# Optimization experiments

Hardware: AMD Instinct MI355X
Metric: run time of the kernel (lower is better)

## Reference

```python
import jax, jax.numpy as jnp
import numpy as np
from jax import lax

B, L, D, C = 4096, 50, 128, 64
V = 100000
H = D // 2  # bidirectional LSTM hidden size; 2*H == emb_dim


def setup_inputs() -> dict:
    key = jax.random.key(0)
    ks = jax.random.split(key, 26)
    f = lambda k, s: jax.random.normal(k, s, dtype=jnp.float32) * 0.05
    return {
        "r_idx": jax.random.randint(ks[0], (B,), 0, V),
        "a_idx": jax.random.randint(ks[1], (B,), 0, V),
        "acc_idx": jax.random.randint(ks[2], (B,), 0, V),
        "rank_q": jax.random.normal(ks[3], (B, L, D), dtype=jnp.float32),
        "rank_q_len": jax.random.randint(ks[4], (B,), 0, L),
        "ru_emb": f(ks[5], (V, D)),
        "au_emb": f(ks[6], (V, D)),
        "Wih_f": f(ks[7], (4 * H, D)), "Whh_f": f(ks[8], (4 * H, H)),
        "bih_f": f(ks[9], (4 * H,)), "bhh_f": f(ks[10], (4 * H,)),
        "Wih_b": f(ks[11], (4 * H, D)), "Whh_b": f(ks[12], (4 * H, H)),
        "bih_b": f(ks[13], (4 * H,)), "bhh_b": f(ks[14], (4 * H,)),
        "conv1_w": f(ks[15], (C, 1, D)), "conv1_b": f(ks[16], (C,)),
        "conv2_w": f(ks[17], (C, 2, D)), "conv2_b": f(ks[18], (C,)),
        "conv3_w": f(ks[19], (C, 3, D)), "conv3_b": f(ks[20], (C,)),
        "fc1_w": f(ks[21], (6,)), "fc1_b": f(ks[22], (1,)),
        "fc2_w": f(ks[23], (C,)), "fc2_b": f(ks[24], (1,)),
    }


def _lstm_dir(x, Wih, Whh, bih, bhh, reverse):
    # x: [B, L, D] -> outputs [B, L, H]; PyTorch gate order i,f,g,o
    b = x.shape[0]
    xs = jnp.swapaxes(x, 0, 1)  # [L, B, D]
    h0 = jnp.zeros((b, Whh.shape[1]), x.dtype)

    def step(carry, xt):
        h, c = carry
        gates = xt @ Wih.T + h @ Whh.T + (bih + bhh)
        i, fg, g, o = jnp.split(gates, 4, axis=-1)
        i = jax.nn.sigmoid(i)
        fg = jax.nn.sigmoid(fg)
        g = jnp.tanh(g)
        o = jax.nn.sigmoid(o)
        c = fg * c + i * g
        h = o * jnp.tanh(c)
        return (h, c), h

    _, ys = lax.scan(step, (h0, h0), xs, reverse=reverse)
    return jnp.swapaxes(ys, 0, 1)


def _score(mat, conv1_w, conv1_b, conv2_w, conv2_b, conv3_w, conv3_b, fc1_w, fc1_b, fc2_w, fc2_b):
    # mat: [B, 3, D]; three tiny conv branches (kernel heights 1/2/3, width=D)
    branches = []
    for w, bias in ((conv1_w, conv1_b), (conv2_w, conv2_b), (conv3_w, conv3_b)):
        k = w.shape[1]
        wins = jnp.stack([mat[:, i:i + k] for i in range(3 - k + 1)], axis=1)  # [B, W, k, D]
        branches.append(jax.nn.relu(jnp.einsum('bwkd,ckd->bcw', wins, w) + bias[None, :, None]))
    s = jnp.concatenate(branches, axis=2)  # [B, C, 6]
    h = jnp.einsum('bcw,w->bc', s, fc1_w) + fc1_b[0]  # fc_new_1: 6 -> 1
    return jnp.einsum('bc,c->b', h, fc2_w) + fc2_b[0]  # fc_new_2: C -> 1


def reference(r_idx, a_idx, acc_idx, rank_q, rank_q_len, ru_emb, au_emb,
              Wih_f, Whh_f, bih_f, bhh_f, Wih_b, Whh_b, bih_b, bhh_b,
              conv1_w, conv1_b, conv2_w, conv2_b, conv3_w, conv3_b,
              fc1_w, fc1_b, fc2_w, fc2_b):
    emb_r = ru_emb[r_idx]
    emb_a = au_emb[a_idx]
    emb_acc = au_emb[acc_idx]
    # bidirectional LSTM over the question sequence
    out_f = _lstm_dir(rank_q, Wih_f, Whh_f, bih_f, bhh_f, reverse=False)
    out_b = _lstm_dir(rank_q, Wih_b, Whh_b, bih_b, bhh_b, reverse=True)
    q_out = jnp.concatenate([out_f, out_b], axis=-1)  # [B, L, D]
    # prepend a zero timestep, then gather per-example at index rank_q_len
    q_pad = jnp.concatenate([jnp.zeros((q_out.shape[0], 1, q_out.shape[2]), q_out.dtype), q_out], axis=1)
    emb_q = q_pad[jnp.arange(q_pad.shape[0]), rank_q_len]  # [B, D]
    low = jnp.stack([emb_r, emb_q, emb_a], axis=1)   # [B, 3, D]
    high = jnp.stack([emb_r, emb_q, emb_acc], axis=1)
    fcp = (conv1_w, conv1_b, conv2_w, conv2_b, conv3_w, conv3_b, fc1_w, fc1_b, fc2_w, fc2_b)
    low_s = _score(low, *fcp)
    high_s = _score(high, *fcp)
    return jnp.sum(low_s - high_s)
```

## Files before the change

### kernel.cpp

```cpp
#include <hip/hip_runtime.h>
#include <hip/hip_bf16.h>

#define LSEQ 50
#define BATCH 4096

typedef __attribute__((ext_vector_type(8))) short bf16x8;
typedef __attribute__((ext_vector_type(4))) float f32x4;

__device__ __forceinline__ unsigned cvtpk(float lo, float hi) {
    unsigned r;
    asm("v_cvt_pk_bf16_f32 %0, %1, %2" : "=v"(r) : "v"(lo), "v"(hi));
    return r;
}
__device__ __forceinline__ bf16x8 pack8(float4 a, float4 b) {
    uint4 u;
    u.x = cvtpk(a.x, a.y); u.y = cvtpk(a.z, a.w);
    u.z = cvtpk(b.x, b.y); u.w = cvtpk(b.z, b.w);
    return __builtin_bit_cast(bf16x8, u);
}
__device__ __forceinline__ float fsigm(float x) {
    return __builtin_amdgcn_rcpf(1.0f + __builtin_amdgcn_exp2f(-1.44269504f * x));
}
__device__ __forceinline__ float ftanh(float x) {
    float e = __builtin_amdgcn_exp2f(2.88539008f * x);
    return 1.0f - 2.0f * __builtin_amdgcn_rcpf(e + 1.0f);
}

__global__ __launch_bounds__(256, 2)
void lstm_kernel(const float* __restrict__ rank_q, const int* __restrict__ qlen,
                 const float* __restrict__ Wih_f, const float* __restrict__ Whh_f,
                 const float* __restrict__ bih_f, const float* __restrict__ bhh_f,
                 const float* __restrict__ Wih_b, const float* __restrict__ Whh_b,
                 const float* __restrict__ bih_b, const float* __restrict__ bhh_b,
                 float* __restrict__ embq)
{
    const int blk = blockIdx.x;
    const int dir = blk >> 8;
    const int b0  = (blk & 255) << 4;
    const int tid = threadIdx.x;
    const int wv  = tid >> 6;
    const int ln  = tid & 63;
    const int lm  = ln & 15;
    const int lq  = ln >> 4;
    const int m   = (wv << 4) + lm;

    const float* Wih = dir ? Wih_b : Wih_f;
    const float* Whh = dir ? Whh_b : Whh_f;
    const float* bih = dir ? bih_b : bih_f;
    const float* bhh = dir ? bhh_b : bhh_f;

    __shared__ __align__(16) unsigned short xbuf[4][16][136];
    __shared__ __align__(16) unsigned short hbuf[2][16][72];

    bf16x8 bfrag[4][6];
    float bias[4];
    #pragma unroll
    for (int j = 0; j < 4; ++j) {
        const int n = (j << 6) + m;
        bias[j] = bih[n] + bhh[n];
        #pragma unroll
        for (int s = 0; s < 6; ++s) {
            const int kb = (s << 5) + (lq << 3);
            const float* src = (s < 4) ? (Wih + n * 128 + kb)
                                       : (Whh + n * 64 + (kb - 128));
            bfrag[j][s] = pack8(*(const float4*)src, *(const float4*)(src + 4));
        }
    }

    int len_e[4];
    #pragma unroll
    for (int r = 0; r < 4; ++r) len_e[r] = qlen[b0 + (lq << 2) + r];

    float cst[4]  = {0.f, 0.f, 0.f, 0.f};
    float qval[4] = {0.f, 0.f, 0.f, 0.f};

    for (int i = tid; i < 16 * 72; i += 256) ((unsigned short*)hbuf)[i] = 0;

    const int se = tid >> 4;
    const int sd = (tid & 15) << 3;
    const int tstep = dir ? -128 : 128;
    const float* gp = rank_q + ((size_t)(b0 + se) * LSEQ + (dir ? LSEQ - 1 : 0)) * 128 + sd;

    float4 p0a = *(const float4*)gp, p0b = *(const float4*)(gp + 4); gp += tstep;
    float4 p1a = *(const float4*)gp, p1b = *(const float4*)(gp + 4); gp += tstep;
    float4 p2a = *(const float4*)gp, p2b = *(const float4*)(gp + 4); gp += tstep;
    float4 p3a = *(const float4*)gp, p3b = *(const float4*)(gp + 4); gp += tstep;
    float4 fa0 = *(const float4*)gp, fa1 = *(const float4*)(gp + 4); gp += tstep;
    float4 fb0 = *(const float4*)gp, fb1 = *(const float4*)(gp + 4); gp += tstep;
    *(bf16x8*)&xbuf[0][se][sd] = pack8(p0a, p0b);
    *(bf16x8*)&xbuf[1][se][sd] = pack8(p1a, p1b);
    *(bf16x8*)&xbuf[2][se][sd] = pack8(p2a, p2b);
    *(bf16x8*)&xbuf[3][se][sd] = pack8(p3a, p3b);
    __syncthreads();

    const int xoff = lm * 136 + (lq << 3);
    const int hoff = lm * 72 + (lq << 3);

    f32x4 accx[4];
    {
        const unsigned short* xb = &xbuf[0][0][0];
        bf16x8 x0 = *(const bf16x8*)(xb + xoff);
        bf16x8 x1 = *(const bf16x8*)(xb + xoff + 32);
        bf16x8 x2 = *(const bf16x8*)(xb + xoff + 64);
        bf16x8 x3 = *(const bf16x8*)(xb + xoff + 96);
        #pragma unroll
        for (int j = 0; j < 4; ++j) {
            f32x4 a = {bias[j], bias[j], bias[j], bias[j]};
            a = __builtin_amdgcn_mfma_f32_16x16x32_bf16(x0, bfrag[j][0], a, 0, 0, 0);
            a = __builtin_amdgcn_mfma_f32_16x16x32_bf16(x1, bfrag[j][1], a, 0, 0, 0);
            a = __builtin_amdgcn_mfma_f32_16x16x32_bf16(x2, bfrag[j][2], a, 0, 0, 0);
            a = __builtin_amdgcn_mfma_f32_16x16x32_bf16(x3, bfrag[j][3], a, 0, 0, 0);
            accx[j] = a;
        }
    }

#define LSTM_BODY(T, FS0, FS1)                                                  \
    {                                                                           \
        const int t  = (T);                                                     \
        const int rb = t & 1, wb = rb ^ 1;                                      \
             \
        if (t + 4 < LSEQ) *(bf16x8*)&xbuf[t & 3][se][sd] = pack8(FS0, FS1);     \
                \
        if (t + 6 < LSEQ) {                                                     \
            FS0 = *(const float4*)gp; FS1 = *(const float4*)(gp + 4);           \
            gp += tstep;                                                        \
        }                                                                       \
                       \
        const unsigned short* hb = &hbuf[rb][0][0];                             \
        bf16x8 ah0 = *(const bf16x8*)(hb + hoff);                               \
        bf16x8 ah1 = *(const bf16x8*)(hb + hoff + 32);                          \
        f32x4 gate[4];                                                          \
        _Pragma("unroll")                                                       \
        for (int j = 0; j < 4; ++j) {                                           \
            f32x4 a = __builtin_amdgcn_mfma_f32_16x16x32_bf16(                  \
                          ah0, bfrag[j][4], accx[j], 0, 0, 0);                  \
            gate[j] = __builtin_amdgcn_mfma_f32_16x16x32_bf16(                  \
                          ah1, bfrag[j][5], a, 0, 0, 0);                        \
        }                                                                       \
          \
        if (t + 1 < LSEQ) {                                                     \
            const unsigned short* xb = &xbuf[(t + 1) & 3][0][0];                \
            bf16x8 x0 = *(const bf16x8*)(xb + xoff);                            \
            bf16x8 x1 = *(const bf16x8*)(xb + xoff + 32);                       \
            bf16x8 x2 = *(const bf16x8*)(xb + xoff + 64);                       \
            bf16x8 x3 = *(const bf16x8*)(xb + xoff + 96);                       \
            _Pragma("unroll")                                                   \
            for (int j = 0; j < 4; ++j) {                                       \
                f32x4 a = {bias[j], bias[j], bias[j], bias[j]};                 \
                a = __builtin_amdgcn_mfma_f32_16x16x32_bf16(x0, bfrag[j][0], a, 0, 0, 0); \
                a = __builtin_amdgcn_mfma_f32_16x16x32_bf16(x1, bfrag[j][1], a, 0, 0, 0); \
                a = __builtin_amdgcn_mfma_f32_16x16x32_bf16(x2, bfrag[j][2], a, 0, 0, 0); \
                a = __builtin_amdgcn_mfma_f32_16x16x32_bf16(x3, bfrag[j][3], a, 0, 0, 0); \
                accx[j] = a;                                                    \
            }                                                                   \
        }                                                                       \
                                  \
        const int tcap = dir ? (LSEQ - 1 - t) : t;                              \
        float hn[4];                                                            \
        _Pragma("unroll")                                                       \
        for (int r = 0; r < 4; ++r) {                                           \
            float ig = fsigm(gate[0][r]);                                       \
            float fg = fsigm(gate[1][r]);                                       \
            float gg = ftanh(gate[2][r]);                                       \
            float og = fsigm(gate[3][r]);                                       \
            float cn = fg * cst[r] + ig * gg;                                   \
            cst[r] = cn;                                                        \
            hn[r] = og * ftanh(cn);                                             \
            if (tcap == len_e[r] - 1) qval[r] = hn[r];                          \
        }                                                                       \
        const unsigned u01 = cvtpk(hn[0], hn[1]);                               \
        const unsigned u23 = cvtpk(hn[2], hn[3]);                               \
        hbuf[wb][(lq << 2) + 0][m] = (unsigned short)u01;                       \
        hbuf[wb][(lq << 2) + 1][m] = (unsigned short)(u01 >> 16);               \
        hbuf[wb][(lq << 2) + 2][m] = (unsigned short)u23;                       \
        hbuf[wb][(lq << 2) + 3][m] = (unsigned short)(u23 >> 16);               \
                    \
        asm volatile("s_waitcnt lgkmcnt(0)\n\ts_barrier" ::: "memory");         \
    }

    for (int i = 0; i < LSEQ / 2; ++i) {
        LSTM_BODY(2 * i,     fa0, fa1)
        LSTM_BODY(2 * i + 1, fb0, fb1)
    }
#undef LSTM_BODY

    #pragma unroll
    for (int r = 0; r < 4; ++r)
        embq[(size_t)(b0 + (lq << 2) + r) * 128 + (dir << 6) + m] = qval[r];
}

__global__ __launch_bounds__(256)
void prep_kernel(const float* __restrict__ c1w, const float* __restrict__ c2w,
                 const float* __restrict__ c3w, float* __restrict__ T)
{
    const int id = blockIdx.x * 256 + threadIdx.x;
    const int m  = id >> 13;
    const int rem = id & 8191;
    const int j  = rem >> 8;
    const int q  = rem & 255;
    const int c  = q >> 2;
    const int d  = (j << 2) + (q & 3);
    const float* src;
    switch (m) {
        case 0:  src = c1w + c * 128 + d;       break;
        case 1:  src = c2w + c * 256 + d;       break;
        case 2:  src = c2w + c * 256 + 128 + d; break;
        case 3:  src = c3w + c * 384 + d;       break;
        case 4:  src = c3w + c * 384 + 128 + d; break;
        default: src = c3w + c * 384 + 256 + d; break;
    }
    T[id] = *src;
}

__global__ __launch_bounds__(256)
void score_kernel(const int* __restrict__ r_idx, const int* __restrict__ a_idx,
                  const int* __restrict__ acc_idx,
                  const float* __restrict__ ru, const float* __restrict__ au,
                  const float* __restrict__ embq, const float* __restrict__ T,
                  const float* __restrict__ c1b, const float* __restrict__ c2b,
                  const float* __restrict__ c3b,
                  const float* __restrict__ fc1w, const float* __restrict__ fc2w,
                  float* __restrict__ diff)
{
    const int tid = threadIdx.x;
    const int wv  = tid >> 6;
    const int c   = tid & 63;
    const int b0  = blockIdx.x << 4;

    __shared__ __align__(16) float emb[64][132];
    {
        const int row = tid & 63;
        const int e   = row >> 2, v = row & 3;
        const int seg = (tid >> 6) << 5;
        const int bb  = b0 + e;
        const float* src = (v == 0) ? ru   + (size_t)r_idx[bb]   * 128 :
                           (v == 1) ? embq + (size_t)bb          * 128 :
                           (v == 2) ? au   + (size_t)a_idx[bb]   * 128 :
                                      au   + (size_t)acc_idx[bb] * 128;
        #pragma unroll
        for (int i = 0; i < 8; ++i) {
            float4 x = *(const float4*)(src + seg + (i << 2));
            *(float4*)&emb[row][seg + (i << 2)] = x;
        }
    }
    __syncthreads();

    float acc[4][9];
    #pragma unroll
    for (int e = 0; e < 4; ++e)
        #pragma unroll
        for (int k = 0; k < 9; ++k) acc[e][k] = 0.f;

    const float4* Tq = (const float4*)T;
    for (int j = 0; j < 32; ++j) {
        const float4* wq = Tq + j * 64 + c;
        const float4 w1  = wq[0];
        const float4 w20 = wq[2048];
        const float4 w21 = wq[4096];
        const float4 w30 = wq[6144];
        const float4 w31 = wq[8192];
        const float4 w32 = wq[10240];
        const int jd = j << 2;
        #pragma unroll
        for (int e = 0; e < 4; ++e) {
            const int br = ((wv << 2) + e) << 2;
            const float4 er = *(const float4*)&emb[br + 0][jd];
            const float4 eq = *(const float4*)&emb[br + 1][jd];
            const float4 ea = *(const float4*)&emb[br + 2][jd];
            const float4 ex = *(const float4*)&emb[br + 3][jd];
            acc[e][0] += w1.x*ea.x  + w1.y*ea.y  + w1.z*ea.z  + w1.w*ea.w;
            acc[e][1] += w1.x*ex.x  + w1.y*ex.y  + w1.z*ex.z  + w1.w*ex.w;
            acc[e][2] += w20.x*eq.x + w20.y*eq.y + w20.z*eq.z + w20.w*eq.w;
            acc[e][3] += w21.x*ea.x + w21.y*ea.y + w21.z*ea.z + w21.w*ea.w;
            acc[e][4] += w21.x*ex.x + w21.y*ex.y + w21.z*ex.z + w21.w*ex.w;
            acc[e][5] += w30.x*er.x + w30.y*er.y + w30.z*er.z + w30.w*er.w;
            acc[e][6] += w31.x*eq.x + w31.y*eq.y + w31.z*eq.z + w31.w*eq.w;
            acc[e][7] += w32.x*ea.x + w32.y*ea.y + w32.z*ea.z + w32.w*ea.w;
            acc[e][8] += w32.x*ex.x + w32.y*ex.y + w32.z*ex.z + w32.w*ex.w;
        }
    }

    const float b1 = c1b[c], b2 = c2b[c], b3 = c3b[c], f2 = fc2w[c];
    const float f12 = fc1w[2], f14 = fc1w[4], f15 = fc1w[5];
    #pragma unroll
    for (int e = 0; e < 4; ++e) {
        const float r1 = fmaxf(acc[e][0] + b1, 0.f) - fmaxf(acc[e][1] + b1, 0.f);
        const float r2 = fmaxf(acc[e][2] + acc[e][3] + b2, 0.f)
                       - fmaxf(acc[e][2] + acc[e][4] + b2, 0.f);
        const float r3 = fmaxf(acc[e][5] + acc[e][6] + acc[e][7] + b3, 0.f)
                       - fmaxf(acc[e][5] + acc[e][6] + acc[e][8] + b3, 0.f);
        float term = f2 * (f12 * r1 + f14 * r2 + f15 * r3);
        #pragma unroll
        for (int off = 32; off; off >>= 1) term += __shfl_down(term, off);
        if (c == 0) diff[b0 + (wv << 2) + e] = term;
    }
}

__global__ void reduce_kernel(const float* __restrict__ diff, float* __restrict__ out)
{
    __shared__ float s[256];
    const int tid = threadIdx.x;
    float v = 0.f;
    for (int i = tid; i < BATCH; i += 256) v += diff[i];
    s[tid] = v;
    __syncthreads();
    for (int st = 128; st > 0; st >>= 1) {
        if (tid < st) s[tid] += s[tid + st];
        __syncthreads();
    }
    if (tid == 0) out[0] = s[0];
}

extern "C" void kernel_launch(void* const* d_in, const int* in_sizes, int n_in,
                              void* d_out, int out_size, void* d_ws, size_t ws_size,
                              hipStream_t stream) {
    (void)in_sizes; (void)n_in; (void)out_size; (void)ws_size;
    const int*   r_idx   = (const int*)d_in[0];
    const int*   a_idx   = (const int*)d_in[1];
    const int*   acc_idx = (const int*)d_in[2];
    const float* rank_q  = (const float*)d_in[3];
    const int*   qlen    = (const int*)d_in[4];
    const float* ru      = (const float*)d_in[5];
    const float* au      = (const float*)d_in[6];
    const float* Wih_f   = (const float*)d_in[7];
    const float* Whh_f   = (const float*)d_in[8];
    const float* bih_f   = (const float*)d_in[9];
    const float* bhh_f   = (const float*)d_in[10];
    const float* Wih_b   = (const float*)d_in[11];
    const float* Whh_b   = (const float*)d_in[12];
    const float* bih_b   = (const float*)d_in[13];
    const float* bhh_b   = (const float*)d_in[14];
    const float* c1w     = (const float*)d_in[15];
    const float* c1b     = (const float*)d_in[16];
    const float* c2w     = (const float*)d_in[17];
    const float* c2b     = (const float*)d_in[18];
    const float* c3w     = (const float*)d_in[19];
    const float* c3b     = (const float*)d_in[20];
    const float* fc1w    = (const float*)d_in[21];
    const float* fc2w    = (const float*)d_in[23];

    float* embq = (float*)d_ws;
    float* diff = embq + (size_t)BATCH * 128;
    float* T    = diff + BATCH;

    prep_kernel<<<192, 256, 0, stream>>>(c1w, c2w, c3w, T);
    lstm_kernel<<<512, 256, 0, stream>>>(rank_q, qlen, Wih_f, Whh_f, bih_f, bhh_f,
                                         Wih_b, Whh_b, bih_b, bhh_b, embq);
    score_kernel<<<BATCH / 16, 256, 0, stream>>>(r_idx, a_idx, acc_idx, ru, au, embq, T,
                                                 c1b, c2b, c3b, fc1w, fc2w, diff);
    reduce_kernel<<<1, 256, 0, stream>>>(diff, (float*)d_out);
}
```

Measured before the change: 98.20 us.

## Halve LSTM batch tile per block to 8 sequences, doubling grid to 1024

Each LSTM block now processes 8 batch rows instead of 16, so the grid grows to 1024 blocks. The MFMA tile stays 16 rows wide, with the upper 8 rows zero-padded and the gate math and stores masked off for lanes that hold no valid row. The aim is to put more independent recurrent chains in flight across the CUs to hide the latency of the serial 50-step dependency. In exchange, half of each MFMA's work is wasted on padding, and the per-block weight loads and conversions are duplicated across twice as many blocks.

```diff
diff --git a/kernel.cpp b/kernel.cpp
--- a/kernel.cpp
+++ b/kernel.cpp
@@ -35,8 +35,8 @@
                  float* __restrict__ embq)
 {
     const int blk = blockIdx.x;
-    const int dir = blk >> 8;
-    const int b0  = (blk & 255) << 4;
+    const int dir = blk >> 9;
+    const int b0  = (blk & 511) << 3;
     const int tid = threadIdx.x;
     const int wv  = tid >> 6;
     const int ln  = tid & 63;
@@ -52,6 +52,9 @@
     __shared__ __align__(16) unsigned short xbuf[4][16][136];
     __shared__ __align__(16) unsigned short hbuf[2][16][72];
 
+    for (int i = tid; i < 4 * 16 * 136; i += 256) ((unsigned short*)xbuf)[i] = 0;
+    for (int i = tid; i < 2 * 16 * 72;  i += 256) ((unsigned short*)hbuf)[i] = 0;
+
     bf16x8 bfrag[4][6];
     float bias[4];
     #pragma unroll
@@ -67,30 +70,38 @@
         }
     }
 
-    int len_e[4];
+    int exq[4], len_e[4];
     #pragma unroll
-    for (int r = 0; r < 4; ++r) len_e[r] = qlen[b0 + (lq << 2) + r];
+    for (int r = 0; r < 4; ++r) {
+        if (lq < 2) { exq[r] = b0 + (lq << 2) + r; len_e[r] = qlen[exq[r]]; }
+        else        { exq[r] = 0; len_e[r] = -1000; }
+    }
 
     float cst[4]  = {0.f, 0.f, 0.f, 0.f};
     float qval[4] = {0.f, 0.f, 0.f, 0.f};
 
-    for (int i = tid; i < 16 * 72; i += 256) ((unsigned short*)hbuf)[i] = 0;
-
     const int se = tid >> 4;
+    const bool sv = (se < 8);
     const int sd = (tid & 15) << 3;
     const int tstep = dir ? -128 : 128;
-    const float* gp = rank_q + ((size_t)(b0 + se) * LSEQ + (dir ? LSEQ - 1 : 0)) * 128 + sd;
-
-    float4 p0a = *(const float4*)gp, p0b = *(const float4*)(gp + 4); gp += tstep;
-    float4 p1a = *(const float4*)gp, p1b = *(const float4*)(gp + 4); gp += tstep;
-    float4 p2a = *(const float4*)gp, p2b = *(const float4*)(gp + 4); gp += tstep;
-    float4 p3a = *(const float4*)gp, p3b = *(const float4*)(gp + 4); gp += tstep;
-    float4 fa0 = *(const float4*)gp, fa1 = *(const float4*)(gp + 4); gp += tstep;
-    float4 fb0 = *(const float4*)gp, fb1 = *(const float4*)(gp + 4); gp += tstep;
-    *(bf16x8*)&xbuf[0][se][sd] = pack8(p0a, p0b);
-    *(bf16x8*)&xbuf[1][se][sd] = pack8(p1a, p1b);
-    *(bf16x8*)&xbuf[2][se][sd] = pack8(p2a, p2b);
-    *(bf16x8*)&xbuf[3][se][sd] = pack8(p3a, p3b);
+    const float* gp = rank_q + ((size_t)(b0 + (sv ? se : 0)) * LSEQ
+                                + (dir ? LSEQ - 1 : 0)) * 128 + sd;
+
+    __syncthreads();
+
+    float4 fa0, fa1, fb0, fb1;
+    if (sv) {
+        float4 p0a = *(const float4*)gp, p0b = *(const float4*)(gp + 4); gp += tstep;
+        float4 p1a = *(const float4*)gp, p1b = *(const float4*)(gp + 4); gp += tstep;
+        float4 p2a = *(const float4*)gp, p2b = *(const float4*)(gp + 4); gp += tstep;
+        float4 p3a = *(const float4*)gp, p3b = *(const float4*)(gp + 4); gp += tstep;
+        fa0 = *(const float4*)gp; fa1 = *(const float4*)(gp + 4); gp += tstep;
+        fb0 = *(const float4*)gp; fb1 = *(const float4*)(gp + 4); gp += tstep;
+        *(bf16x8*)&xbuf[0][se][sd] = pack8(p0a, p0b);
+        *(bf16x8*)&xbuf[1][se][sd] = pack8(p1a, p1b);
+        *(bf16x8*)&xbuf[2][se][sd] = pack8(p2a, p2b);
+        *(bf16x8*)&xbuf[3][se][sd] = pack8(p3a, p3b);
+    }
     __syncthreads();
 
     const int xoff = lm * 136 + (lq << 3);
@@ -119,9 +130,9 @@
         const int t  = (T);                                                     \
         const int rb = t & 1, wb = rb ^ 1;                                      \
              \
-        if (t + 4 < LSEQ) *(bf16x8*)&xbuf[t & 3][se][sd] = pack8(FS0, FS1);     \
-                \
-        if (t + 6 < LSEQ) {                                                     \
+        if (sv && t + 4 < LSEQ) *(bf16x8*)&xbuf[t & 3][se][sd] = pack8(FS0, FS1); \
+                                         \
+        if (sv && t + 6 < LSEQ) {                                               \
             FS0 = *(const float4*)gp; FS1 = *(const float4*)(gp + 4);           \
             gp += tstep;                                                        \
         }                                                                       \
@@ -154,26 +165,28 @@
                 accx[j] = a;                                                    \
             }                                                                   \
         }                                                                       \
-                                  \
-        const int tcap = dir ? (LSEQ - 1 - t) : t;                              \
-        float hn[4];                                                            \
-        _Pragma("unroll")                                                       \
-        for (int r = 0; r < 4; ++r) {                                           \
-            float ig = fsigm(gate[0][r]);                                       \
-            float fg = fsigm(gate[1][r]);                                       \
-            float gg = ftanh(gate[2][r]);                                       \
-            float og = fsigm(gate[3][r]);                                       \
-            float cn = fg * cst[r] + ig * gg;                                   \
-            cst[r] = cn;                                                        \
-            hn[r] = og * ftanh(cn);                                             \
-            if (tcap == len_e[r] - 1) qval[r] = hn[r];                          \
+                  \
+        if (lq < 2) {                                                           \
+            const int tcap = dir ? (LSEQ - 1 - t) : t;                          \
+            float hn[4];                                                        \
+            _Pragma("unroll")                                                   \
+            for (int r = 0; r < 4; ++r) {                                       \
+                float ig = fsigm(gate[0][r]);                                   \
+                float fg = fsigm(gate[1][r]);                                   \
+                float gg = ftanh(gate[2][r]);                                   \
+                float og = fsigm(gate[3][r]);                                   \
+                float cn = fg * cst[r] + ig * gg;                               \
+                cst[r] = cn;                                                    \
+                hn[r] = og * ftanh(cn);                                         \
+                if (tcap == len_e[r] - 1) qval[r] = hn[r];                      \
+            }                                                                   \
+            const unsigned u01 = cvtpk(hn[0], hn[1]);                           \
+            const unsigned u23 = cvtpk(hn[2], hn[3]);                           \
+            hbuf[wb][(lq << 2) + 0][m] = (unsigned short)u01;                   \
+            hbuf[wb][(lq << 2) + 1][m] = (unsigned short)(u01 >> 16);           \
+            hbuf[wb][(lq << 2) + 2][m] = (unsigned short)u23;                   \
+            hbuf[wb][(lq << 2) + 3][m] = (unsigned short)(u23 >> 16);           \
         }                                                                       \
-        const unsigned u01 = cvtpk(hn[0], hn[1]);                               \
-        const unsigned u23 = cvtpk(hn[2], hn[3]);                               \
-        hbuf[wb][(lq << 2) + 0][m] = (unsigned short)u01;                       \
-        hbuf[wb][(lq << 2) + 1][m] = (unsigned short)(u01 >> 16);               \
-        hbuf[wb][(lq << 2) + 2][m] = (unsigned short)u23;                       \
-        hbuf[wb][(lq << 2) + 3][m] = (unsigned short)(u23 >> 16);               \
                     \
         asm volatile("s_waitcnt lgkmcnt(0)\n\ts_barrier" ::: "memory");         \
     }
@@ -184,9 +197,11 @@
     }
 #undef LSTM_BODY
 
-    #pragma unroll
-    for (int r = 0; r < 4; ++r)
-        embq[(size_t)(b0 + (lq << 2) + r) * 128 + (dir << 6) + m] = qval[r];
+    if (lq < 2) {
+        #pragma unroll
+        for (int r = 0; r < 4; ++r)
+            embq[(size_t)exq[r] * 128 + (dir << 6) + m] = qval[r];
+    }
 }
 
 __global__ __launch_bounds__(256)
@@ -344,8 +359,8 @@
     float* T    = diff + BATCH;
 
     prep_kernel<<<192, 256, 0, stream>>>(c1w, c2w, c3w, T);
-    lstm_kernel<<<512, 256, 0, stream>>>(rank_q, qlen, Wih_f, Whh_f, bih_f, bhh_f,
-                                         Wih_b, Whh_b, bih_b, bhh_b, embq);
+    lstm_kernel<<<1024, 256, 0, stream>>>(rank_q, qlen, Wih_f, Whh_f, bih_f, bhh_f,
+                                          Wih_b, Whh_b, bih_b, bhh_b, embq);
     score_kernel<<<BATCH / 16, 256, 0, stream>>>(r_idx, a_idx, acc_idx, ru, au, embq, T,
                                                  c1b, c2b, c3b, fc1w, fc2w, diff);
     reduce_kernel<<<1, 256, 0, stream>>>(diff, (float*)d_out);
```

Measured after the change: 154.2 us. +57.0%, slower.
